# Kernel tuning notes

Hardware: AMD Instinct MI355X
Metric: run time of the kernel (lower is better)

The kernel has to match this reference:

```python
import jax, jax.numpy as jnp
import numpy as np

FORGET_BIAS = 1.0  # TF BasicLSTMCell default

B, T, D, H = 64, 1024, 300, 512


def setup_inputs() -> dict:
    key = jax.random.key(0)
    k1, k2, k3 = jax.random.split(key, 3)
    essays = jax.random.normal(k1, (B, T, D), dtype=jnp.float32)
    # TF BasicLSTMCell: single kernel [D+H, 4H], gate order (i, j, f, o)
    W_lstm = jax.random.normal(k2, (D + H, 4 * H), dtype=jnp.float32) * 0.05
    b_lstm = jnp.zeros((4 * H,), dtype=jnp.float32)
    W_dense = jax.random.normal(k3, (H, 1), dtype=jnp.float32) * 0.05
    b_dense = jnp.zeros((1,), dtype=jnp.float32)
    return {"essays": essays, "W_lstm": W_lstm, "b_lstm": b_lstm,
            "W_dense": W_dense, "b_dense": b_dense}


def _lstm_scan(essays, W_lstm, b_lstm):
    # Precompute input projection for all timesteps: [B,T,4H]
    Wx, Wh = W_lstm[:D], W_lstm[D:]
    x_proj = jnp.einsum('btd,dg->btg', essays, Wx) + b_lstm

    def step(carry, xp):
        c, h = carry
        gates = xp + h @ Wh  # [B,4H]
        i, j, f, o = jnp.split(gates, 4, axis=-1)
        new_c = c * jax.nn.sigmoid(f + FORGET_BIAS) + jax.nn.sigmoid(i) * jnp.tanh(j)
        new_h = jnp.tanh(new_c) * jax.nn.sigmoid(o)
        return (new_c, new_h), new_h

    init = (jnp.zeros((essays.shape[0], H), essays.dtype),
            jnp.zeros((essays.shape[0], H), essays.dtype))
    _, hs = jax.lax.scan(step, init, jnp.swapaxes(x_proj, 0, 1))  # hs: [T,B,H]
    return jnp.swapaxes(hs, 0, 1)  # [B,T,H]


def reference(essays, W_lstm, b_lstm, W_dense, b_dense):
    lstm_out = _lstm_scan(essays, W_lstm, b_lstm)      # [B,T,H]
    mot = jnp.mean(lstm_out, axis=1)                   # mean-over-time pooling [B,H]
    preds = jax.nn.sigmoid(mot @ W_dense + b_dense)    # [B,1]
    return preds.reshape(-1)                           # [B]
```

## Files before the change

kernel.cpp:

```cpp
#include <hip/hip_runtime.h>
#include <hip/hip_bf16.h>
#include <stdint.h>

#define B_   64
#define T_   1024
#define D_   300
#define H_   512
#define G4H  2048
#define KP   320

typedef __attribute__((ext_vector_type(8))) short short8;
typedef __attribute__((ext_vector_type(4))) float f32x4;
typedef unsigned long long ull;

__device__ __forceinline__ unsigned short f2bf(float v) {
    __hip_bfloat16 h = __float2bfloat16(v);
    return *reinterpret_cast<unsigned short*>(&h);
}
__device__ __forceinline__ float bf2f(unsigned short u) {
    return __uint_as_float(((unsigned)u) << 16);
}
__device__ __forceinline__ float sigm(float x) { return 1.f / (1.f + __expf(-x)); }
__device__ __forceinline__ float tanhfast(float x) {
    float e = __expf(2.f * x);
    return 1.f - 2.f / (e + 1.f);
}

#define ASYNC16(g, l)                                                        \
    __builtin_amdgcn_global_load_lds(                                        \
        (const __attribute__((address_space(1))) void*)(g),                  \
        (__attribute__((address_space(3))) void*)(l), 16, 0, 0)

__global__ void cvt_essays(const float* __restrict__ es, unsigned short* __restrict__ Ab) {
    unsigned i = blockIdx.x * 256u + threadIdx.x;
    unsigned row = i / KP;
    unsigned col = i - row * KP;
    float v = (col < D_) ? es[(size_t)row * D_ + col] : 0.f;
    Ab[i] = f2bf(v);
}

__global__ void cvt_misc(const float* __restrict__ Wl, unsigned short* __restrict__ Bt,
                         unsigned short* __restrict__ hbuf, unsigned int* __restrict__ cnt) {
    unsigned i = blockIdx.x * 256u + threadIdx.x;
    {
        unsigned n = i / KP, k = i - n * KP;
        float v = (k < D_) ? Wl[(size_t)k * G4H + n] : 0.f;
        Bt[i] = f2bf(v);
    }
    if (i < 2u * 64u * 512u) hbuf[i] = 0;
    if (i < 256u) cnt[i] = 0u;
}

__global__ __launch_bounds__(256) void gemm_xp(
    const unsigned short* __restrict__ Ab,
    const unsigned short* __restrict__ Bt,
    const float* __restrict__ bias,
    unsigned short* __restrict__ Cb)
{
    __shared__ __align__(16) unsigned short Al[128 * 32];
    __shared__ __align__(16) unsigned short Bl[128 * 32];
    const int tid = threadIdx.x;
    const int w = tid >> 6, lane = tid & 63;
    const int ln = lane & 15, q = lane >> 4;
    const int bx = blockIdx.x;
    const int m0 = (bx >> 4) * 128;
    const int n0 = (bx & 15) * 128;
    const int wr = w >> 1, wc = w & 1;

    f32x4 acc[4][4];
#pragma unroll
    for (int i = 0; i < 4; i++)
#pragma unroll
        for (int j = 0; j < 4; j++) acc[i][j] = (f32x4){0.f, 0.f, 0.f, 0.f};

    for (int k0 = 0; k0 < KP; k0 += 32) {
#pragma unroll
        for (int it = 0; it < 2; ++it) {
            int s = it * 4 + w;
            int c = s * 64 + lane;
            int r = c >> 2;
            int ko = (c & 3) * 8;
            ASYNC16(Ab + (size_t)(m0 + r) * KP + k0 + ko, &Al[s * 512]);
            ASYNC16(Bt + (size_t)(n0 + r) * KP + k0 + ko, &Bl[s * 512]);
        }
        __syncthreads();
        short8 af[4], bf[4];
#pragma unroll
        for (int mt = 0; mt < 4; ++mt)
            af[mt] = *(const short8*)&Al[(wr * 64 + mt * 16 + ln) * 32 + q * 8];
#pragma unroll
        for (int nt = 0; nt < 4; ++nt)
            bf[nt] = *(const short8*)&Bl[(wc * 64 + nt * 16 + ln) * 32 + q * 8];
#pragma unroll
        for (int mt = 0; mt < 4; ++mt)
#pragma unroll
            for (int nt = 0; nt < 4; ++nt)
                acc[mt][nt] = __builtin_amdgcn_mfma_f32_16x16x32_bf16(af[mt], bf[nt], acc[mt][nt], 0, 0, 0);
        __syncthreads();
    }
#pragma unroll
    for (int mt = 0; mt < 4; ++mt) {
#pragma unroll
        for (int nt = 0; nt < 4; ++nt) {
            int col = n0 + wc * 64 + nt * 16 + ln;
            float bb = bias[col];
#pragma unroll
            for (int r = 0; r < 4; ++r) {
                int row = m0 + wr * 64 + mt * 16 + q * 4 + r;
                Cb[(size_t)row * G4H + col] = f2bf(acc[mt][nt][r] + bb);
            }
        }
    }
}

__global__ __launch_bounds__(256, 1) void lstm_rec(
    const float* __restrict__ Wl,
    const unsigned short* __restrict__ xp,
    unsigned short* __restrict__ hbuf,
    float* __restrict__ hmean,
    unsigned int* __restrict__ cnt)
{
    __shared__ __align__(16) unsigned short WhT[64 * 520];
    __shared__ __align__(16) unsigned short hl[16 * 520];
    __shared__ float gbuf[4 * 16 * 17];

    const int tid = threadIdx.x;
    const int bid = blockIdx.x;
    const int g   = bid >> 5;
    const int j0  = (bid & 31) * 16;
    const int bg  = g * 16;
    const int wv  = tid >> 6, lane = tid & 63, ln = lane & 15, q = lane >> 4;

    {
        const int c  = tid & 63;
        const int gc = (c >> 4) * 512 + j0 + (c & 15);
        for (int k = tid >> 6; k < 512; k += 4)
            WhT[c * 520 + k] = f2bf(Wl[(size_t)(300 + k) * G4H + gc]);
    }
    const int b = tid >> 4;
    const int j = tid & 15;
    float c_st = 0.f, hsum = 0.f;
    unsigned int* myc = cnt + g * 64;

    const unsigned short* xbase = xp + (size_t)(bg + b) * T_ * G4H + j0 + j;
    unsigned short xc0, xc1, xc2, xc3, xn0, xn1, xn2, xn3;
    {
        const unsigned short* q_ = xbase;
        xc0 = q_[0]; xc1 = q_[512]; xc2 = q_[1024]; xc3 = q_[1536];
    }

    unsigned long long* const hl8 = (unsigned long long*)hl;

    for (int t = 0; t < T_; ++t) {
        {
            const ull* hb8 = (const ull*)(hbuf + (size_t)(t & 1) * 32768 + (size_t)bg * 512);
#pragma unroll
            for (int i = 0; i < 8; ++i) {
                int c = tid + (i << 8);
                ull v = __hip_atomic_load(hb8 + c, __ATOMIC_RELAXED, __HIP_MEMORY_SCOPE_AGENT);
                hl8[(c >> 7) * 130 + (c & 127)] = v;
            }
        }
        __syncthreads();

        f32x4 acc = (f32x4){0.f, 0.f, 0.f, 0.f};
#pragma unroll
        for (int kk = 0; kk < 16; ++kk) {
            short8 a  = *(const short8*)&hl[ln * 520 + kk * 32 + q * 8];
            short8 bb = *(const short8*)&WhT[(wv * 16 + ln) * 520 + kk * 32 + q * 8];
            acc = __builtin_amdgcn_mfma_f32_16x16x32_bf16(a, bb, acc, 0, 0, 0);
        }
#pragma unroll
        for (int r = 0; r < 4; ++r)
            gbuf[wv * 272 + (q * 4 + r) * 17 + ln] = acc[r];

        {
            const unsigned short* q_ = xbase + (size_t)((t + 1 < T_) ? t + 1 : t) * G4H;
            xn0 = q_[0]; xn1 = q_[512]; xn2 = q_[1024]; xn3 = q_[1536];
        }
        __syncthreads();

        float ai  = gbuf[0 * 272 + b * 17 + j] + bf2f(xc0);
        float aj  = gbuf[1 * 272 + b * 17 + j] + bf2f(xc1);
        float af_ = gbuf[2 * 272 + b * 17 + j] + bf2f(xc2);
        float ao  = gbuf[3 * 272 + b * 17 + j] + bf2f(xc3);
        float si = sigm(ai), tj = tanhfast(aj);
        float sf = sigm(af_ + 1.0f), so = sigm(ao);
        c_st = c_st * sf + si * tj;
        float h = tanhfast(c_st) * so;
        hsum += h;
        xc0 = xn0; xc1 = xn1; xc2 = xn2; xc3 = xn3;

        {
            unsigned u0 = f2bf(h);
            unsigned u1 = __shfl_down(u0, 1);
            unsigned u2 = __shfl_down(u0, 2);
            unsigned u3 = __shfl_down(u0, 3);
            if ((j & 3) == 0) {
                ull pk = (ull)(u0 | (u1 << 16)) | ((ull)(u2 | (u3 << 16)) << 32);
                ull* dst = (ull*)(hbuf + (size_t)((t + 1) & 1) * 32768
                                  + (size_t)(bg + b) * 512 + j0 + j);
                __hip_atomic_store(dst, pk, __ATOMIC_RELAXED, __HIP_MEMORY_SCOPE_AGENT);
            }
        }

        if (t < T_ - 1) {
            __syncthreads();
            if (tid == 0) {
                __hip_atomic_fetch_add(myc, 1u, __ATOMIC_RELAXED, __HIP_MEMORY_SCOPE_AGENT);
                unsigned target = 32u * (unsigned)(t + 1);
                while (__hip_atomic_load(myc, __ATOMIC_RELAXED, __HIP_MEMORY_SCOPE_AGENT) < target) {}
            }
            __syncthreads();
        }
    }
    hmean[(size_t)(bg + b) * 512 + j0 + j] = hsum * (1.f / 1024.f);
}

__global__ void dense_out(const float* __restrict__ hmean, const float* __restrict__ Wd,
                          const float* __restrict__ bd, float* __restrict__ out) {
    int bb = blockIdx.x;
    int lane = threadIdx.x;
    float p = 0.f;
    for (int e = lane; e < H_; e += 64) p += hmean[(size_t)bb * H_ + e] * Wd[e];
#pragma unroll
    for (int off = 32; off; off >>= 1) p += __shfl_down(p, off);
    if (lane == 0) out[bb] = 1.f / (1.f + __expf(-(p + bd[0])));
}

extern "C" void kernel_launch(void* const* d_in, const int* in_sizes, int n_in,
                              void* d_out, int out_size, void* d_ws, size_t ws_size,
                              hipStream_t stream) {
    const float* essays  = (const float*)d_in[0];
    const float* W_lstm  = (const float*)d_in[1];
    const float* b_lstm  = (const float*)d_in[2];
    const float* W_dense = (const float*)d_in[3];
    const float* b_dense = (const float*)d_in[4];
    float* out = (float*)d_out;

    char* ws = (char*)d_ws;
    unsigned short* xp   = (unsigned short*)(ws);
    unsigned short* Ab   = (unsigned short*)(ws + 268435456ull);
    unsigned short* Bt   = (unsigned short*)(ws + 310378496ull);
    unsigned short* hbuf = (unsigned short*)(ws + 311689216ull);
    float*          hm   = (float*)(ws + 311820288ull);
    unsigned int*   cnt  = (unsigned int*)(ws + 311951360ull);

    hipLaunchKernelGGL(cvt_essays, dim3(81920), dim3(256), 0, stream, essays, Ab);
    hipLaunchKernelGGL(cvt_misc,   dim3(2560),  dim3(256), 0, stream, W_lstm, Bt, hbuf, cnt);
    hipLaunchKernelGGL(gemm_xp,    dim3(8192),  dim3(256), 0, stream, Ab, Bt, b_lstm, xp);
    hipLaunchKernelGGL(lstm_rec,   dim3(128),   dim3(256), 0, stream, W_lstm, xp, hbuf, hm, cnt);
    hipLaunchKernelGGL(dense_out,  dim3(64),    dim3(64),  0, stream, hm, W_dense, b_dense, out);
}
```

Baseline: 4.119 ms.

## Halve recurrent blocks and replace atomic counter barrier with per-block flags

The recurrent kernel now uses 64 blocks, each owning 32 hidden units instead of 16. Each thread handles two units and does two MFMAs per k-step. The shared fetch-add counter barrier is replaced by per-block progress flags that one wavefront polls with a ballot. The next-step input projection load is issued before the h-buffer read. A separate kernel pre-transposes Wh to bf16 so blocks can load it with vector copies. The goal is less contention and latency in the per-timestep grid sync. The cost is more work per block per step and an extra launch.

After: 4.824 ms. 1.17x slower.

```diff
diff --git a/kernel.cpp b/kernel.cpp
--- a/kernel.cpp
+++ b/kernel.cpp
@@ -17,8 +17,8 @@
     __hip_bfloat16 h = __float2bfloat16(v);
     return *reinterpret_cast<unsigned short*>(&h);
 }
-__device__ __forceinline__ float bf2f(unsigned short u) {
-    return __uint_as_float(((unsigned)u) << 16);
+__device__ __forceinline__ float bf2f(unsigned u) {
+    return __uint_as_float(u << 16);
 }
 __device__ __forceinline__ float sigm(float x) { return 1.f / (1.f + __expf(-x)); }
 __device__ __forceinline__ float tanhfast(float x) {
@@ -40,7 +40,7 @@
 }
 
 __global__ void cvt_misc(const float* __restrict__ Wl, unsigned short* __restrict__ Bt,
-                         unsigned short* __restrict__ hbuf, unsigned int* __restrict__ cnt) {
+                         unsigned short* __restrict__ hbuf, unsigned int* __restrict__ flags) {
     unsigned i = blockIdx.x * 256u + threadIdx.x;
     {
         unsigned n = i / KP, k = i - n * KP;
@@ -48,7 +48,13 @@
         Bt[i] = f2bf(v);
     }
     if (i < 2u * 64u * 512u) hbuf[i] = 0;
-    if (i < 256u) cnt[i] = 0u;
+    if (i < 256u) flags[i] = 0u;
+}
+
+__global__ void cvt_wh(const float* __restrict__ Wl, unsigned short* __restrict__ WhTg) {
+    unsigned i = blockIdx.x * 256u + threadIdx.x;
+    unsigned gc = i & 2047u, k = i >> 11;
+    WhTg[(size_t)gc * 512 + k] = f2bf(Wl[(size_t)(300 + k) * G4H + gc]);
 }
 
 __global__ __launch_bounds__(256) void gemm_xp(
@@ -114,46 +120,62 @@
 }
 
 __global__ __launch_bounds__(256, 1) void lstm_rec(
-    const float* __restrict__ Wl,
+    const unsigned short* __restrict__ WhTg,
     const unsigned short* __restrict__ xp,
     unsigned short* __restrict__ hbuf,
     float* __restrict__ hmean,
-    unsigned int* __restrict__ cnt)
+    unsigned int* __restrict__ flags)
 {
-    __shared__ __align__(16) unsigned short WhT[64 * 520];
+    __shared__ __align__(16) unsigned short WhT[128 * 520];
     __shared__ __align__(16) unsigned short hl[16 * 520];
-    __shared__ float gbuf[4 * 16 * 17];
+    __shared__ float gbuf[4][16][35];
 
     const int tid = threadIdx.x;
     const int bid = blockIdx.x;
-    const int g   = bid >> 5;
-    const int j0  = (bid & 31) * 16;
-    const int bg  = g * 16;
-    const int wv  = tid >> 6, lane = tid & 63, ln = lane & 15, q = lane >> 4;
-
-    {
-        const int c  = tid & 63;
-        const int gc = (c >> 4) * 512 + j0 + (c & 15);
-        for (int k = tid >> 6; k < 512; k += 4)
-            WhT[c * 520 + k] = f2bf(Wl[(size_t)(300 + k) * G4H + gc]);
-    }
-    const int b = tid >> 4;
-    const int j = tid & 15;
-    float c_st = 0.f, hsum = 0.f;
-    unsigned int* myc = cnt + g * 64;
-
-    const unsigned short* xbase = xp + (size_t)(bg + b) * T_ * G4H + j0 + j;
-    unsigned short xc0, xc1, xc2, xc3, xn0, xn1, xn2, xn3;
-    {
-        const unsigned short* q_ = xbase;
-        xc0 = q_[0]; xc1 = q_[512]; xc2 = q_[1024]; xc3 = q_[1536];
-    }
-
-    unsigned long long* const hl8 = (unsigned long long*)hl;
+    const int g     = bid >> 4;
+    const int slice = bid & 15;
+    const int j0    = slice * 32;
+    const int bg    = g * 16;
+    const int wv = tid >> 6, lane = tid & 63, ln = lane & 15, q = lane >> 4;
+
+    for (int ch = tid; ch < 128 * 64; ch += 256) {
+        int c = ch >> 6, off = (ch & 63) * 8;
+        int gc = (c >> 5) * 512 + j0 + (c & 31);
+        *(uint4*)&WhT[c * 520 + off] = *(const uint4*)&WhTg[(size_t)gc * 512 + off];
+    }
+
+    const int b  = tid >> 4;
+    const int jj = tid & 15;
+    float c0 = 0.f, c1 = 0.f, hs0 = 0.f, hs1 = 0.f;
+
+    const unsigned short* xrow = xp + (size_t)(bg + b) * T_ * G4H + j0 + 2 * jj;
+    unsigned xc0 = *(const unsigned*)(xrow);
+    unsigned xc1 = *(const unsigned*)(xrow + 512);
+    unsigned xc2 = *(const unsigned*)(xrow + 1024);
+    unsigned xc3 = *(const unsigned*)(xrow + 1536);
+    unsigned xn0 = 0, xn1 = 0, xn2 = 0, xn3 = 0;
+
+    ull* const hl8 = (ull*)hl;
+    const unsigned int* fl = flags + g * 64 + (lane & 15);
 
     for (int t = 0; t < T_; ++t) {
+        if (t > 0) {
+            const unsigned tgt = (unsigned)t;
+            while (true) {
+                unsigned v = __hip_atomic_load(fl, __ATOMIC_RELAXED, __HIP_MEMORY_SCOPE_AGENT);
+                if (__ballot((int)(v >= tgt)) == ~0ull) break;
+            }
+            xc0 = xn0; xc1 = xn1; xc2 = xn2; xc3 = xn3;
+        }
+        if (t + 1 < T_) {
+            const unsigned short* xr = xrow + (size_t)(t + 1) * G4H;
+            xn0 = *(const unsigned*)(xr);
+            xn1 = *(const unsigned*)(xr + 512);
+            xn2 = *(const unsigned*)(xr + 1024);
+            xn3 = *(const unsigned*)(xr + 1536);
+        }
         {
-            const ull* hb8 = (const ull*)(hbuf + (size_t)(t & 1) * 32768 + (size_t)bg * 512);
+            const ull* hb8 = (const ull*)(hbuf + (size_t)(t & 1) * 32768) + (size_t)bg * 128;
 #pragma unroll
             for (int i = 0; i < 8; ++i) {
                 int c = tid + (i << 8);
@@ -163,58 +185,50 @@
         }
         __syncthreads();
 
-        f32x4 acc = (f32x4){0.f, 0.f, 0.f, 0.f};
+        f32x4 a0 = (f32x4){0.f, 0.f, 0.f, 0.f};
+        f32x4 a1 = (f32x4){0.f, 0.f, 0.f, 0.f};
 #pragma unroll
         for (int kk = 0; kk < 16; ++kk) {
-            short8 a  = *(const short8*)&hl[ln * 520 + kk * 32 + q * 8];
-            short8 bb = *(const short8*)&WhT[(wv * 16 + ln) * 520 + kk * 32 + q * 8];
-            acc = __builtin_amdgcn_mfma_f32_16x16x32_bf16(a, bb, acc, 0, 0, 0);
-        }
-#pragma unroll
-        for (int r = 0; r < 4; ++r)
-            gbuf[wv * 272 + (q * 4 + r) * 17 + ln] = acc[r];
-
-        {
-            const unsigned short* q_ = xbase + (size_t)((t + 1 < T_) ? t + 1 : t) * G4H;
-            xn0 = q_[0]; xn1 = q_[512]; xn2 = q_[1024]; xn3 = q_[1536];
-        }
-        __syncthreads();
-
-        float ai  = gbuf[0 * 272 + b * 17 + j] + bf2f(xc0);
-        float aj  = gbuf[1 * 272 + b * 17 + j] + bf2f(xc1);
-        float af_ = gbuf[2 * 272 + b * 17 + j] + bf2f(xc2);
-        float ao  = gbuf[3 * 272 + b * 17 + j] + bf2f(xc3);
-        float si = sigm(ai), tj = tanhfast(aj);
-        float sf = sigm(af_ + 1.0f), so = sigm(ao);
-        c_st = c_st * sf + si * tj;
-        float h = tanhfast(c_st) * so;
-        hsum += h;
-        xc0 = xn0; xc1 = xn1; xc2 = xn2; xc3 = xn3;
-
-        {
-            unsigned u0 = f2bf(h);
-            unsigned u1 = __shfl_down(u0, 1);
-            unsigned u2 = __shfl_down(u0, 2);
-            unsigned u3 = __shfl_down(u0, 3);
-            if ((j & 3) == 0) {
-                ull pk = (ull)(u0 | (u1 << 16)) | ((ull)(u2 | (u3 << 16)) << 32);
-                ull* dst = (ull*)(hbuf + (size_t)((t + 1) & 1) * 32768
-                                  + (size_t)(bg + b) * 512 + j0 + j);
-                __hip_atomic_store(dst, pk, __ATOMIC_RELAXED, __HIP_MEMORY_SCOPE_AGENT);
-            }
-        }
+            short8 av = *(const short8*)&hl[ln * 520 + kk * 32 + q * 8];
+            short8 b0 = *(const short8*)&WhT[(wv * 32 + ln) * 520 + kk * 32 + q * 8];
+            short8 b1 = *(const short8*)&WhT[(wv * 32 + 16 + ln) * 520 + kk * 32 + q * 8];
+            a0 = __builtin_amdgcn_mfma_f32_16x16x32_bf16(av, b0, a0, 0, 0, 0);
+            a1 = __builtin_amdgcn_mfma_f32_16x16x32_bf16(av, b1, a1, 0, 0, 0);
+        }
+#pragma unroll
+        for (int r = 0; r < 4; ++r) {
+            gbuf[wv][q * 4 + r][ln]      = a0[r];
+            gbuf[wv][q * 4 + r][16 + ln] = a1[r];
+        }
+        __syncthreads();
+
+        float ai0 = gbuf[0][b][2 * jj] + bf2f(xc0 & 0xffffu);
+        float ai1 = gbuf[0][b][2 * jj + 1] + bf2f(xc0 >> 16);
+        float aj0 = gbuf[1][b][2 * jj] + bf2f(xc1 & 0xffffu);
+        float aj1 = gbuf[1][b][2 * jj + 1] + bf2f(xc1 >> 16);
+        float af0 = gbuf[2][b][2 * jj] + bf2f(xc2 & 0xffffu);
+        float af1 = gbuf[2][b][2 * jj + 1] + bf2f(xc2 >> 16);
+        float ao0 = gbuf[3][b][2 * jj] + bf2f(xc3 & 0xffffu);
+        float ao1 = gbuf[3][b][2 * jj + 1] + bf2f(xc3 >> 16);
+        c0 = c0 * sigm(af0 + 1.0f) + sigm(ai0) * tanhfast(aj0);
+        c1 = c1 * sigm(af1 + 1.0f) + sigm(ai1) * tanhfast(aj1);
+        float h0 = tanhfast(c0) * sigm(ao0);
+        float h1 = tanhfast(c1) * sigm(ao1);
+        unsigned pk = (unsigned)f2bf(h0) | ((unsigned)f2bf(h1) << 16);
+        __hip_atomic_store(
+            (unsigned*)(hbuf + (size_t)((t + 1) & 1) * 32768 + (size_t)(bg + b) * 512 + j0 + 2 * jj),
+            pk, __ATOMIC_RELAXED, __HIP_MEMORY_SCOPE_AGENT);
+        hs0 += h0; hs1 += h1;
 
         if (t < T_ - 1) {
             __syncthreads();
-            if (tid == 0) {
-                __hip_atomic_fetch_add(myc, 1u, __ATOMIC_RELAXED, __HIP_MEMORY_SCOPE_AGENT);
-                unsigned target = 32u * (unsigned)(t + 1);
-                while (__hip_atomic_load(myc, __ATOMIC_RELAXED, __HIP_MEMORY_SCOPE_AGENT) < target) {}
-            }
-            __syncthreads();
-        }
-    }
-    hmean[(size_t)(bg + b) * 512 + j0 + j] = hsum * (1.f / 1024.f);
+            if (tid == 0)
+                __hip_atomic_store(flags + g * 64 + slice, (unsigned)(t + 1),
+                                   __ATOMIC_RELAXED, __HIP_MEMORY_SCOPE_AGENT);
+        }
+    }
+    float2 hm2 = make_float2(hs0 * (1.f / 1024.f), hs1 * (1.f / 1024.f));
+    *(float2*)&hmean[(size_t)(bg + b) * 512 + j0 + 2 * jj] = hm2;
 }
 
 __global__ void dense_out(const float* __restrict__ hmean, const float* __restrict__ Wd,
@@ -242,13 +256,15 @@
     unsigned short* xp   = (unsigned short*)(ws);
     unsigned short* Ab   = (unsigned short*)(ws + 268435456ull);
     unsigned short* Bt   = (unsigned short*)(ws + 310378496ull);
-    unsigned short* hbuf = (unsigned short*)(ws + 311689216ull);
-    float*          hm   = (float*)(ws + 311820288ull);
-    unsigned int*   cnt  = (unsigned int*)(ws + 311951360ull);
+    unsigned short* WhTg = (unsigned short*)(ws + 311689216ull);
+    unsigned short* hbuf = (unsigned short*)(ws + 313786368ull);
+    float*          hm   = (float*)(ws + 313917440ull);
+    unsigned int*   flg  = (unsigned int*)(ws + 314048512ull);
 
     hipLaunchKernelGGL(cvt_essays, dim3(81920), dim3(256), 0, stream, essays, Ab);
-    hipLaunchKernelGGL(cvt_misc,   dim3(2560),  dim3(256), 0, stream, W_lstm, Bt, hbuf, cnt);
+    hipLaunchKernelGGL(cvt_misc,   dim3(2560),  dim3(256), 0, stream, W_lstm, Bt, hbuf, flg);
+    hipLaunchKernelGGL(cvt_wh,     dim3(4096),  dim3(256), 0, stream, W_lstm, WhTg);
     hipLaunchKernelGGL(gemm_xp,    dim3(8192),  dim3(256), 0, stream, Ab, Bt, b_lstm, xp);
-    hipLaunchKernelGGL(lstm_rec,   dim3(128),   dim3(256), 0, stream, W_lstm, xp, hbuf, hm, cnt);
+    hipLaunchKernelGGL(lstm_rec,   dim3(64),    dim3(256), 0, stream, WhTg, xp, hbuf, hm, flg);
     hipLaunchKernelGGL(dense_out,  dim3(64),    dim3(64),  0, stream, hm, W_dense, b_dense, out);
 }
```
